# Optimization experiments

Measured on AMD Instinct MI355X. Metric: run time of the kernel, lower is better.

The kernel has to match this reference:

```python
import jax, jax.numpy as jnp
import numpy as np

N = 25000   # nodes of type 'window'
E = 200000  # edges per relation
H = 512     # hidden_channels
OUT = 250   # out_channels
L = 4       # num_layers
R = 3       # relations: near, close, sim


def setup_inputs() -> dict:
    key = jax.random.key(0)
    ks = jax.random.split(key, 8)
    s = 1.0 / np.sqrt(H).astype(np.float32)
    x = jax.random.normal(ks[0], (N, H), jnp.float32)
    W_pre = jax.random.normal(ks[1], (H, H), jnp.float32) * s
    W_post = jax.random.normal(ks[2], (H, H), jnp.float32) * s
    Wl = jax.random.normal(ks[3], (L, R, H, H), jnp.float32) * s   # SAGEConv lin_l (neighbors)
    Wr = jax.random.normal(ks[4], (L, R, H, H), jnp.float32) * s   # SAGEConv lin_r (root)
    bl = jnp.zeros((L, R, H), jnp.float32)                         # lin_l bias
    W_out = jax.random.normal(ks[5], (H, OUT), jnp.float32) * s
    b_out = jnp.zeros((OUT,), jnp.float32)
    edges = jax.random.randint(ks[6], (R, 2, E), 0, N, jnp.int32)  # [rel, (src,dst), E]
    return dict(x=x, W_pre=W_pre, W_post=W_post, Wl=Wl, Wr=Wr, bl=bl,
                W_out=W_out, b_out=b_out, edges=edges)


def _leaky(v):
    return jnp.where(v >= 0, v, 0.2 * v)


def reference(x, W_pre, W_post, Wl, Wr, bl, W_out, b_out, edges):
    # pretransform + post_transform: leaky(leaky(x @ Wpre) @ Wpost)
    h = _leaky(_leaky(x @ W_pre) @ W_post)

    # per-relation destination in-degree (constant across layers)
    inv_deg = []
    for r in range(R):
        cnt = jax.ops.segment_sum(jnp.ones((E,), h.dtype), edges[r, 1], num_segments=N)
        inv_deg.append(1.0 / jnp.maximum(cnt, 1.0))  # [N]

    for l in range(L):
        acc = jnp.zeros_like(h)
        for r in range(R):
            src, dst = edges[r, 0], edges[r, 1]
            # mean aggregation of neighbor features over destinations
            agg = jax.ops.segment_sum(h[src], dst, num_segments=N) * inv_deg[r][:, None]
            # SAGEConv: lin_l(agg) + lin_r(x_root)
            acc = acc + (agg @ Wl[l, r] + bl[l, r] + h @ Wr[l, r])
        # HeteroConv aggr='mean' across relations, then LeakyReLU(0.2)
        h = _leaky(acc / R)

    return h @ W_out + b_out
```

## Files before the change

kernel.cpp:

```cpp
#include <hip/hip_runtime.h>

#define N_ 25000
#define E_ 200000
#define H_ 512
#define OUT_ 250
#define WSZ (H_ * H_)

typedef unsigned short u16;
typedef unsigned int u32;
typedef __bf16 bf16x8 __attribute__((ext_vector_type(8)));
typedef float f32x4 __attribute__((ext_vector_type(4)));

__device__ __forceinline__ u16 f2b(float f) {
  union { float f; u32 u; } c; c.f = f;
  u32 r = c.u + 0x7FFFu + ((c.u >> 16) & 1u);
  return (u16)(r >> 16);
}
__device__ __forceinline__ void async16(const void* g, void* l) {
  __builtin_amdgcn_global_load_lds((__attribute__((address_space(1))) void*)g,
                                   (__attribute__((address_space(3))) void*)l, 16, 0, 0);
}

__global__ void conv_x(const float* __restrict__ x, u16* __restrict__ xb, int n4) {
  int i = blockIdx.x * 256 + threadIdx.x;
  if (i >= n4) return;
  const float4 v = *(const float4*)(x + (size_t)i * 4);
  ushort4 o;
  o.x = f2b(v.x); o.y = f2b(v.y); o.z = f2b(v.z); o.w = f2b(v.w);
  *(ushort4*)(xb + (size_t)i * 4) = o;
}

__global__ void prep_wt(const float* __restrict__ Wpre, const float* __restrict__ Wpost,
                        const float* __restrict__ Wl, const float* __restrict__ Wr,
                        u16* __restrict__ WT) {
  __shared__ u16 tile[32][33];
  const int id = blockIdx.z;
  const int tx = blockIdx.x, ty = blockIdx.y;
  const int x = threadIdx.x, y = threadIdx.y;
  const float* src = nullptr;
  bool sum3 = false;
  if (id == 0) src = Wpre;
  else if (id == 1) src = Wpost;
  else {
    int li = (id - 2) >> 2, ri = (id - 2) & 3;
    if (ri < 3) src = Wl + (size_t)(li * 3 + ri) * WSZ;
    else { sum3 = true; src = Wr + (size_t)(li * 3) * WSZ; }
  }
#pragma unroll
  for (int i = 0; i < 4; ++i) {
    int row = ty * 32 + y + i * 8;
    int col = tx * 32 + x;
    float f = src[(size_t)row * 512 + col];
    if (sum3) f += src[WSZ + (size_t)row * 512 + col] + src[2 * WSZ + (size_t)row * 512 + col];
    tile[y + i * 8][x] = f2b(f);
  }
  __syncthreads();
#pragma unroll
  for (int i = 0; i < 4; ++i) {
    WT[(size_t)id * WSZ + (tx * 32 + y + i * 8) * 512 + ty * 32 + x] = tile[x][y + i * 8];
  }
}

__global__ void prep_wout(const float* __restrict__ Wout, u16* __restrict__ WoutT) {
  __shared__ u16 tile[32][33];
  const int tx = blockIdx.x, ty = blockIdx.y;
  const int x = threadIdx.x, y = threadIdx.y;
#pragma unroll
  for (int i = 0; i < 4; ++i) {
    int row = ty * 32 + y + i * 8;
    int col = tx * 32 + x;
    tile[y + i * 8][x] = (col < OUT_) ? f2b(Wout[(size_t)row * OUT_ + col]) : (u16)0;
  }
  __syncthreads();
#pragma unroll
  for (int i = 0; i < 4; ++i) {
    WoutT[(tx * 32 + y + i * 8) * 512 + ty * 32 + x] = tile[x][y + i * 8];
  }
}

__global__ void prep_bias(const float* __restrict__ bl, const float* __restrict__ bout,
                          float* __restrict__ blSum, float* __restrict__ bOutF) {
  int t = threadIdx.x;
  for (int l = 0; l < 4; ++l)
    blSum[l * 512 + t] = bl[(l * 3 + 0) * 512 + t] + bl[(l * 3 + 1) * 512 + t] +
                         bl[(l * 3 + 2) * 512 + t];
  if (t < 256) bOutF[t] = (t < OUT_) ? bout[t] : 0.0f;
}

__global__ void hist_kernel(const int* __restrict__ edges, int* __restrict__ counts) {
  int idx = blockIdx.x * 256 + threadIdx.x;
  if (idx >= 3 * E_) return;
  int r = idx / E_, e = idx - r * E_;
  int dst = edges[r * 2 * E_ + E_ + e];
  atomicAdd(&counts[r * N_ + dst], 1);
}

__global__ __launch_bounds__(1024) void scan_kernel(const int* __restrict__ counts,
                                                    int* __restrict__ rowptr,
                                                    int* __restrict__ cursor) {
  const int r = blockIdx.x;
  const int* cnt = counts + r * N_;
  int* rp = rowptr + r * (N_ + 1);
  int* cur = cursor + r * N_;
  __shared__ int wsum[2][16];
  const int tid = threadIdx.x;
  const int wv = tid >> 6, lane = tid & 63;
  int roff = 0;
  int par = 0;
  for (int base = 0; base < N_; base += 1024, par ^= 1) {
    int v = (base + tid < N_) ? cnt[base + tid] : 0;
    int inc = v;
#pragma unroll
    for (int d = 1; d < 64; d <<= 1) {
      int t = __shfl_up(inc, d, 64);
      if (lane >= d) inc += t;
    }
    if (lane == 63) wsum[par][wv] = inc;
    __syncthreads();
    if (tid < 16) {
      int s = wsum[par][tid];
#pragma unroll
      for (int d = 1; d < 16; d <<= 1) {
        int t = __shfl_up(s, d, 64);
        if (tid >= d) s += t;
      }
      wsum[par][tid] = s;
    }
    __syncthreads();
    int woff = (wv == 0) ? 0 : wsum[par][wv - 1];
    int excl = roff + woff + inc - v;
    if (base + tid < N_) { rp[base + tid] = excl; cur[base + tid] = excl; }
    roff += wsum[par][15];
  }
  if (tid == 0) rp[N_] = roff;
}

__global__ void scatter_kernel(const int* __restrict__ edges, int* __restrict__ cursor,
                               int* __restrict__ colidx) {
  int idx = blockIdx.x * 256 + threadIdx.x;
  if (idx >= 3 * E_) return;
  int r = idx / E_, e = idx - r * E_;
  int src = edges[r * 2 * E_ + e];
  int dst = edges[r * 2 * E_ + E_ + e];
  int pos = atomicAdd(&cursor[r * N_ + dst], 1);
  colidx[r * E_ + pos] = src;
}

__global__ void invdeg_kernel(const int* __restrict__ counts, float* __restrict__ invdeg) {
  int idx = blockIdx.x * 256 + threadIdx.x;
  if (idx >= 3 * N_) return;
  invdeg[idx] = 1.0f / fmaxf((float)counts[idx], 1.0f);
}

__device__ __forceinline__ void acc8(float* acc, uint4 u) {
  union { u32 u; float f; } c;
  c.u = u.x << 16;          acc[0] += c.f;
  c.u = u.x & 0xffff0000u;  acc[1] += c.f;
  c.u = u.y << 16;          acc[2] += c.f;
  c.u = u.y & 0xffff0000u;  acc[3] += c.f;
  c.u = u.z << 16;          acc[4] += c.f;
  c.u = u.z & 0xffff0000u;  acc[5] += c.f;
  c.u = u.w << 16;          acc[6] += c.f;
  c.u = u.w & 0xffff0000u;  acc[7] += c.f;
}

__global__ __launch_bounds__(256) void agg_kernel(const u16* __restrict__ h,
                                                  const int* __restrict__ rowptr,
                                                  const int* __restrict__ colidx,
                                                  const float* __restrict__ invdeg,
                                                  u16* __restrict__ agg) {
  const int w = threadIdx.x >> 6, lane = threadIdx.x & 63;
  const int node = blockIdx.x * 4 + w;
  const int r = blockIdx.y;
  if (node >= N_) return;
  const int* rp = rowptr + r * (N_ + 1);
  const int* ci = colidx + r * E_;
  const u16* hb = h + lane * 8;
  const int s = rp[node], e = rp[node + 1];
  float acc[8] = {0.f, 0.f, 0.f, 0.f, 0.f, 0.f, 0.f, 0.f};
  int p = s;
  for (; p + 8 <= e; p += 8) {
    int sx[8];
#pragma unroll
    for (int q = 0; q < 8; ++q) sx[q] = ci[p + q];
    uint4 u[8];
#pragma unroll
    for (int q = 0; q < 8; ++q) u[q] = *(const uint4*)(hb + (size_t)sx[q] * 512);
#pragma unroll
    for (int q = 0; q < 8; ++q) acc8(acc, u[q]);
  }
  for (; p + 2 <= e; p += 2) {
    int s0 = ci[p], s1 = ci[p + 1];
    const uint4 u0 = *(const uint4*)(hb + (size_t)s0 * 512);
    const uint4 u1 = *(const uint4*)(hb + (size_t)s1 * 512);
    acc8(acc, u0); acc8(acc, u1);
  }
  if (p < e) acc8(acc, *(const uint4*)(hb + (size_t)ci[p] * 512));
  const float sc = invdeg[r * N_ + node];
  uint4 o;
  o.x = (u32)f2b(acc[0] * sc) | ((u32)f2b(acc[1] * sc) << 16);
  o.y = (u32)f2b(acc[2] * sc) | ((u32)f2b(acc[3] * sc) << 16);
  o.z = (u32)f2b(acc[4] * sc) | ((u32)f2b(acc[5] * sc) << 16);
  o.w = (u32)f2b(acc[6] * sc) | ((u32)f2b(acc[7] * sc) << 16);
  *(uint4*)(agg + ((size_t)r * N_ + node) * 512 + lane * 8) = o;
}

#define BM 128
#define BN 128
#define BK 64
__global__ __launch_bounds__(256, 4) void gemm_mfma(
    const u16* __restrict__ A0, const u16* __restrict__ A1,
    const u16* __restrict__ A2, const u16* __restrict__ A3,
    const u16* __restrict__ Bt, const float* __restrict__ bias,
    u16* __restrict__ C, float* __restrict__ Cf,
    int M, int G, int ldc, int Nreal, float scale, int leaky) {
  __shared__ __align__(16) u16 As[BM * BK];
  __shared__ __align__(16) u16 Bs[BN * BK];
  const int tid = threadIdx.x;
  const int lane = tid & 63;
  const int w = tid >> 6;

  const int gx = gridDim.x;
  const int lin = blockIdx.y * gx + blockIdx.x;
  const int gsz = gx * 8;
  const int grp = lin / gsz;
  const int l = lin - grp * gsz;
  const int rem = (int)gridDim.y - grp * 8;
  int by, bx;
  if (rem >= 8) { by = grp * 8 + (l & 7); bx = l >> 3; }
  else          { by = grp * 8 + l % rem; bx = l / rem; }
  const int row0 = by * BM;
  const int col0 = bx * BN;

  int aOff[4], bOff[4], lOff[4];
#pragma unroll
  for (int i = 0; i < 4; ++i) {
    const int idx = i * 256 + tid;
    const int arow = idx >> 3;
    const int c = (idx & 7) ^ (arow & 7);
    int grow = row0 + arow; if (grow >= M) grow = M - 1;
    aOff[i] = grow * 512 + c * 8;
    bOff[i] = (col0 + arow) * 512 + c * 8;
    lOff[i] = idx * 16;
  }

  const int lm = lane & 15;
  const int lk = lane >> 4;
  const int x0 = ((lk ^ (lane & 7)) << 3);
  const int x1 = (((4 + lk) ^ (lane & 7)) << 3);
  const int wm = (w >> 1) * 64;
  const int wn = (w & 1) * 64;
  int aRow[4], bRow[4];
#pragma unroll
  for (int i = 0; i < 4; ++i) {
    aRow[i] = (wm + i * 16 + lm) * BK;
    bRow[i] = (wn + i * 16 + lm) * BK;
  }

  f32x4 acc[4][4] = {};

  for (int g = 0; g < G; ++g) {
    const u16* Ag = (g == 0) ? A0 : (g == 1) ? A1 : (g == 2) ? A2 : A3;
    const u16* Bg = Bt + ((size_t)g << 18);
#pragma unroll
    for (int ki = 0; ki < 8; ++ki) {
      const u16* Ab = Ag + ki * 64;
      const u16* Bb = Bg + ki * 64;
#pragma unroll
      for (int i = 0; i < 4; ++i) {
        async16(Ab + aOff[i], (char*)As + lOff[i]);
        async16(Bb + bOff[i], (char*)Bs + lOff[i]);
      }
      __syncthreads();
      {
        bf16x8 af[4], bfr[4];
#pragma unroll
        for (int i = 0; i < 4; ++i) {
          af[i]  = *(const bf16x8*)((const char*)As + ((aRow[i] + x0) << 1));
          bfr[i] = *(const bf16x8*)((const char*)Bs + ((bRow[i] + x0) << 1));
        }
#pragma unroll
        for (int i = 0; i < 4; ++i)
#pragma unroll
          for (int j = 0; j < 4; ++j)
            acc[i][j] = __builtin_amdgcn_mfma_f32_16x16x32_bf16(af[i], bfr[j], acc[i][j], 0, 0, 0);
#pragma unroll
        for (int i = 0; i < 4; ++i) {
          af[i]  = *(const bf16x8*)((const char*)As + ((aRow[i] + x1) << 1));
          bfr[i] = *(const bf16x8*)((const char*)Bs + ((bRow[i] + x1) << 1));
        }
#pragma unroll
        for (int i = 0; i < 4; ++i)
#pragma unroll
          for (int j = 0; j < 4; ++j)
            acc[i][j] = __builtin_amdgcn_mfma_f32_16x16x32_bf16(af[i], bfr[j], acc[i][j], 0, 0, 0);
      }
      __syncthreads();
    }
  }

  const int crow_base = row0 + wm + (lk << 2);
  const int ccol_base = col0 + wn + lm;
#pragma unroll
  for (int i = 0; i < 4; ++i) {
#pragma unroll
    for (int j = 0; j < 4; ++j) {
      const int ccol = ccol_base + j * 16;
      const float badd = bias ? bias[ccol] : 0.0f;
#pragma unroll
      for (int rg = 0; rg < 4; ++rg) {
        const int crow = crow_base + i * 16 + rg;
        if (crow < M && ccol < Nreal) {
          float v = (acc[i][j][rg] + badd) * scale;
          if (leaky) v = (v >= 0.0f) ? v : 0.2f * v;
          if (Cf) Cf[(size_t)crow * ldc + ccol] = v;
          else    C[(size_t)crow * ldc + ccol] = f2b(v);
        }
      }
    }
  }
}

extern "C" void kernel_launch(void* const* d_in, const int* in_sizes, int n_in,
                              void* d_out, int out_size, void* d_ws, size_t ws_size,
                              hipStream_t stream) {
  const float* x     = (const float*)d_in[0];
  const float* Wpre  = (const float*)d_in[1];
  const float* Wpost = (const float*)d_in[2];
  const float* Wl    = (const float*)d_in[3];
  const float* Wr    = (const float*)d_in[4];
  const float* bl    = (const float*)d_in[5];
  const float* Wout  = (const float*)d_in[6];
  const float* bout  = (const float*)d_in[7];
  const int*   edges = (const int*)d_in[8];
  float* out = (float*)d_out;

  char* p = (char*)d_ws;
  auto alloc = [&](size_t b) { void* q = (void*)p; p += (b + 255) & ~(size_t)255; return q; };
  u16*   WT     = (u16*)alloc((size_t)18 * WSZ * 2);
  u16*   WoutT  = (u16*)alloc((size_t)256 * 512 * 2);
  float* blSum  = (float*)alloc(4 * 512 * 4);
  float* bOutF  = (float*)alloc(256 * 4);
  u16*   hA     = (u16*)alloc((size_t)N_ * 512 * 2);
  u16*   hB     = (u16*)alloc((size_t)N_ * 512 * 2);
  u16*   aggb   = (u16*)alloc((size_t)3 * N_ * 512 * 2);
  int*   counts = (int*)alloc(3 * N_ * 4);
  float* invdeg = (float*)alloc(3 * N_ * 4);
  int*   rowptr = (int*)alloc(3 * (N_ + 1) * 4);
  int*   cursor = (int*)alloc(3 * N_ * 4);
  int*   colidx = (int*)alloc((size_t)3 * E_ * 4);
  u16*   xb     = aggb;

  hipMemsetAsync(counts, 0, 3 * N_ * 4, stream);
  conv_x<<<(N_ * 512 / 4 + 255) / 256, 256, 0, stream>>>(x, xb, N_ * 512 / 4);
  prep_wt<<<dim3(16, 16, 18), dim3(32, 8), 0, stream>>>(Wpre, Wpost, Wl, Wr, WT);
  prep_wout<<<dim3(8, 16), dim3(32, 8), 0, stream>>>(Wout, WoutT);
  prep_bias<<<1, 512, 0, stream>>>(bl, bout, blSum, bOutF);
  hist_kernel<<<(3 * E_ + 255) / 256, 256, 0, stream>>>(edges, counts);
  scan_kernel<<<3, 1024, 0, stream>>>(counts, rowptr, cursor);
  scatter_kernel<<<(3 * E_ + 255) / 256, 256, 0, stream>>>(edges, cursor, colidx);
  invdeg_kernel<<<(3 * N_ + 255) / 256, 256, 0, stream>>>(counts, invdeg);

  const dim3 blk(256);
  const dim3 g512(512 / 128, (N_ + 127) / 128);
  gemm_mfma<<<g512, blk, 0, stream>>>(xb, xb, xb, xb, WT, nullptr, hA, nullptr,
                                      N_, 1, 512, 512, 1.0f, 1);
  gemm_mfma<<<g512, blk, 0, stream>>>(hA, hA, hA, hA, WT + WSZ, nullptr, hB, nullptr,
                                      N_, 1, 512, 512, 1.0f, 1);

  u16* hc = hB; u16* hn = hA;
  for (int l = 0; l < 4; ++l) {
    agg_kernel<<<dim3(N_ / 4, 3), blk, 0, stream>>>(hc, rowptr, colidx, invdeg, aggb);
    gemm_mfma<<<g512, blk, 0, stream>>>(aggb, aggb + (size_t)N_ * 512, aggb + (size_t)2 * N_ * 512, hc,
                                        WT + (size_t)(2 + 4 * l) * WSZ, blSum + l * 512, hn, nullptr,
                                        N_, 4, 512, 512, 1.0f / 3.0f, 1);
    u16* t = hc; hc = hn; hn = t;
  }
  const dim3 gout(256 / 128, (N_ + 127) / 128);
  gemm_mfma<<<gout, blk, 0, stream>>>(hc, hc, hc, hc, WoutT, bOutF, nullptr, out,
                                      N_, 1, OUT_, OUT_, 1.0f, 0);
}
```

Measured before the change: 936.6 us.

## Split aggregation across feature chunks with eight nodes per wavefront

The mean-aggregation kernel now gives each wavefront eight destination nodes. Each node is handled by eight lanes covering one 64-feature chunk, and blockIdx.x encodes both the chunk and a group of 32 nodes. The 8-way unrolled gather loop is replaced by a one-deep software-pipelined loop. The aim is to spread uneven degree across more independent work items and keep only one chunk of h hot per block, at the cost of fewer outstanding loads per lane and more blocks re-reading the same column indices.

```diff
diff --git a/kernel.cpp b/kernel.cpp
--- a/kernel.cpp
+++ b/kernel.cpp
@@ -169,40 +169,38 @@
                                                   const int* __restrict__ colidx,
                                                   const float* __restrict__ invdeg,
                                                   u16* __restrict__ agg) {
-  const int w = threadIdx.x >> 6, lane = threadIdx.x & 63;
-  const int node = blockIdx.x * 4 + w;
+  const int chunk = blockIdx.x & 7;
+  const int nb = blockIdx.x >> 3;
   const int r = blockIdx.y;
+  const int wv = threadIdx.x >> 6;
+  const int lane = threadIdx.x & 63;
+  const int grp = lane >> 3, sub = lane & 7;
+  const int node = nb * 32 + wv * 8 + grp;
   if (node >= N_) return;
   const int* rp = rowptr + r * (N_ + 1);
   const int* ci = colidx + r * E_;
-  const u16* hb = h + lane * 8;
+  const u16* hb = h + chunk * 64 + sub * 8;
   const int s = rp[node], e = rp[node + 1];
   float acc[8] = {0.f, 0.f, 0.f, 0.f, 0.f, 0.f, 0.f, 0.f};
   int p = s;
-  for (; p + 8 <= e; p += 8) {
-    int sx[8];
-#pragma unroll
-    for (int q = 0; q < 8; ++q) sx[q] = ci[p + q];
-    uint4 u[8];
-#pragma unroll
-    for (int q = 0; q < 8; ++q) u[q] = *(const uint4*)(hb + (size_t)sx[q] * 512);
-#pragma unroll
-    for (int q = 0; q < 8; ++q) acc8(acc, u[q]);
-  }
-  for (; p + 2 <= e; p += 2) {
-    int s0 = ci[p], s1 = ci[p + 1];
-    const uint4 u0 = *(const uint4*)(hb + (size_t)s0 * 512);
-    const uint4 u1 = *(const uint4*)(hb + (size_t)s1 * 512);
-    acc8(acc, u0); acc8(acc, u1);
-  }
-  if (p < e) acc8(acc, *(const uint4*)(hb + (size_t)ci[p] * 512));
+  if (p < e) {
+    int src = ci[p];
+    uint4 u = *(const uint4*)(hb + (size_t)src * 512);
+    for (++p; p < e; ++p) {
+      int src2 = ci[p];
+      uint4 u2 = *(const uint4*)(hb + (size_t)src2 * 512);
+      acc8(acc, u);
+      u = u2;
+    }
+    acc8(acc, u);
+  }
   const float sc = invdeg[r * N_ + node];
   uint4 o;
   o.x = (u32)f2b(acc[0] * sc) | ((u32)f2b(acc[1] * sc) << 16);
   o.y = (u32)f2b(acc[2] * sc) | ((u32)f2b(acc[3] * sc) << 16);
   o.z = (u32)f2b(acc[4] * sc) | ((u32)f2b(acc[5] * sc) << 16);
   o.w = (u32)f2b(acc[6] * sc) | ((u32)f2b(acc[7] * sc) << 16);
-  *(uint4*)(agg + ((size_t)r * N_ + node) * 512 + lane * 8) = o;
+  *(uint4*)(agg + ((size_t)r * N_ + node) * 512 + chunk * 64 + sub * 8) = o;
 }
 
 #define BM 128
@@ -363,6 +361,7 @@
 
   const dim3 blk(256);
   const dim3 g512(512 / 128, (N_ + 127) / 128);
+  const dim3 gagg(((N_ + 31) / 32) * 8, 3);
   gemm_mfma<<<g512, blk, 0, stream>>>(xb, xb, xb, xb, WT, nullptr, hA, nullptr,
                                       N_, 1, 512, 512, 1.0f, 1);
   gemm_mfma<<<g512, blk, 0, stream>>>(hA, hA, hA, hA, WT + WSZ, nullptr, hB, nullptr,
@@ -370,7 +369,7 @@
 
   u16* hc = hB; u16* hn = hA;
   for (int l = 0; l < 4; ++l) {
-    agg_kernel<<<dim3(N_ / 4, 3), blk, 0, stream>>>(hc, rowptr, colidx, invdeg, aggb);
+    agg_kernel<<<gagg, blk, 0, stream>>>(hc, rowptr, colidx, invdeg, aggb);
     gemm_mfma<<<g512, blk, 0, stream>>>(aggb, aggb + (size_t)N_ * 512, aggb + (size_t)2 * N_ * 512, hc,
                                         WT + (size_t)(2 + 4 * l) * WSZ, blSum + l * 512, hn, nullptr,
                                         N_, 4, 512, 512, 1.0f / 3.0f, 1);
```

After: 867.6 us. 1.08x faster.
